# Kernel tuning notes

Measured on AMD Instinct MI355X. Metric: run time of the kernel, lower is better.

The kernel has to match this reference:

```python
import jax, jax.numpy as jnp
import numpy as np

NH = 32          # num_attention_heads
LAYER_ID = 3     # per-layer scaling coeff = LAYER_ID + 1
SQ, B, H = 1024, 2, 4096
MEM_LEN = 1024
HD = H // NH


def setup_inputs() -> dict:
    key = jax.random.key(0)
    ks = jax.random.split(key, 6)
    hidden_states = jax.random.normal(ks[0], (SQ, B, H), dtype=jnp.float32)
    mem = jax.random.normal(ks[1], (B, MEM_LEN, 2 * NH * HD), dtype=jnp.float32) * 0.5
    qkv_w = jax.random.normal(ks[2], (3 * H, H), dtype=jnp.float32) * 0.02
    qkv_b = jax.random.normal(ks[3], (3 * H,), dtype=jnp.float32) * 0.02
    dense_w = jax.random.normal(ks[4], (H, H), dtype=jnp.float32) * 0.02
    dense_b = jax.random.normal(ks[5], (H,), dtype=jnp.float32) * 0.02
    # causal mask over new tokens; mem positions fully visible. True = masked.
    kv = MEM_LEN + SQ
    mask = ((jnp.arange(kv)[None, :] - MEM_LEN) > jnp.arange(SQ)[:, None])
    mask = mask[None, None, :, :]  # [1,1,sq,kv]
    # position ids of new tokens continue after the mem cache: [b, sq]
    position_ids = jnp.broadcast_to(MEM_LEN + jnp.arange(SQ, dtype=jnp.int64), (B, SQ))
    return {"hidden_states": hidden_states, "mask": mask, "position_ids": position_ids,
            "mem": mem, "qkv_w": qkv_w, "qkv_b": qkv_b, "dense_w": dense_w, "dense_b": dense_b}


def _rotate_half(x):
    x1, x2 = jnp.split(x, 2, axis=-1)
    return jnp.concatenate((-x2, x1), axis=-1)


def _rotary_tables(max_pos):
    inv_freq = 1.0 / (10000.0 ** (jnp.arange(0, HD, 2, dtype=jnp.float32) / HD))
    t = jnp.arange(max_pos, dtype=jnp.float32)
    freqs = jnp.einsum('i,j->ij', t, inv_freq)          # [L, HD/2]
    emb = jnp.concatenate((freqs, freqs), axis=-1)      # [L, HD]
    return jnp.cos(emb), jnp.sin(emb)


def reference(hidden_states, mask, position_ids, mem, qkv_w, qkv_b, dense_w, dense_b):
    sq, b, h = hidden_states.shape
    coeff = float(LAYER_ID + 1)
    # QKV projection: [sq,b,3H] -> [sq,b,nh,3*hd] -> split
    mixed = jnp.einsum('sbh,oh->sbo', hidden_states, qkv_w) + qkv_b
    mixed = mixed.reshape(sq, b, NH, 3 * HD)
    q, k, v = jnp.split(mixed, 3, axis=-1)              # each [sq,b,nh,hd]
    # rotary embedding with position indices (position_ids: [b,sq] -> [sq,b])
    pos = position_ids.T                                 # [sq,b]
    cos_t, sin_t = _rotary_tables(MEM_LEN + SQ)          # table up to max pos + 1
    cos = cos_t[pos][:, :, None, :]                      # [sq,b,1,hd]
    sin = sin_t[pos][:, :, None, :]
    q = q * cos + _rotate_half(q) * sin
    k = k * cos + _rotate_half(k) * sin
    # mem-KV concat: mem [b, mem_len, 2*nh*hd] -> memk/memv [mem_len,b,nh,hd]
    m = mem.reshape(b, MEM_LEN, 2, NH, HD).transpose(2, 1, 0, 3, 4)
    k = jnp.concatenate((m[0], k), axis=0)               # [kv,b,nh,hd]
    v = jnp.concatenate((m[1], v), axis=0)
    # per-layer scaled attention scores
    q = q / (np.sqrt(HD) * coeff)
    scores = jnp.einsum('sbnh,tbnh->bnst', q, k)         # [b,nh,sq,kv]
    scores = jnp.where(mask, -10000.0, scores)
    scores = scores * coeff
    probs = jax.nn.softmax(scores, axis=-1)
    ctx = jnp.einsum('bnst,tbnh->sbnh', probs, v).reshape(sq, b, h)
    out = jnp.einsum('sbh,oh->sbo', ctx, dense_w) + dense_b
    return out
```

## Files before the change

### kernel.cpp

```cpp
#include <hip/hip_runtime.h>


typedef __attribute__((ext_vector_type(4))) float f32x4;
typedef __attribute__((ext_vector_type(8))) short bf16x8;
typedef unsigned short u16;

#define SQ   1024
#define BSZ  2
#define H    4096
#define NH   32
#define HD   128
#define MEML 1024
#define KV   2048

__device__ __forceinline__ u16 f32_to_bf16(float f) {
  union { float f; unsigned int u; } v; v.f = f;
  unsigned int r = v.u + 0x7FFFu + ((v.u >> 16) & 1u);
  return (u16)(r >> 16);
}
__device__ __forceinline__ float bf16_to_f32(u16 x) {
  union { unsigned int u; float f; } v; v.u = ((unsigned int)x) << 16; return v.f;
}

__device__ __forceinline__ void gload_lds16(const void* g, void* l) {
  __builtin_amdgcn_global_load_lds((const __attribute__((address_space(1))) void*)g,
                                   (__attribute__((address_space(3))) void*)l, 16, 0, 0);
}

__global__ __launch_bounds__(256) void conv_bf16(const float* __restrict__ in,
                                                 u16* __restrict__ out, int n4) {
  int idx = blockIdx.x * 256 + threadIdx.x;
  if (idx < n4) {
    float4 v = ((const float4*)in)[idx];
    ushort4 o;
    o.x = f32_to_bf16(v.x); o.y = f32_to_bf16(v.y);
    o.z = f32_to_bf16(v.z); o.w = f32_to_bf16(v.w);
    ((ushort4*)out)[idx] = o;
  }
}

__global__ __launch_bounds__(256) void rope_tables(float* __restrict__ cost, float* __restrict__ sint) {
  int idx = blockIdx.x * 256 + threadIdx.x;
  int s = idx >> 6, j = idx & 63;
  float inv = powf(10000.0f, -(float)j / 64.0f);
  float ang = (float)(MEML + s) * inv;
  cost[idx] = cosf(ang);
  sint[idx] = sinf(ang);
}

template <typename OUT_T, int NF>
__global__ __launch_bounds__(512, 2) void gemmT(const u16* __restrict__ A, const u16* __restrict__ B,
                                                const float* __restrict__ bias, OUT_T* __restrict__ C,
                                                int N, int K) {
  constexpr int WN = NF * 16;
  constexpr int NH0 = (NF + 1) / 2;
  constexpr int SB2 = NF - (NF >> 1);
  __shared__ char lds[2][32768 + NF * 8192];
  const int tid = threadIdx.x;
  const int lane = tid & 63;
  const int w = tid >> 6;
  const int wm = w >> 2, wn = w & 3;
  const int rl = lane & 15, cg = lane >> 4;
  const int m0 = blockIdx.y * 256, n0 = blockIdx.x * (NF * 64);
  const int nt = K >> 6;

  const int srow = tid >> 3;
  const int scb = ((tid & 7) << 4) ^ ((srow & 7) << 4);

  auto stage_a = [&](int tile, int ua) {
    if (tile >= nt) return;
    gload_lds16((const char*)(A + (size_t)(m0 + ua * 64 + srow) * K + (size_t)tile * 64) + scb,
                lds[tile & 1] + ua * 8192 + tid * 16);
  };
  auto stage_b = [&](int tile, int ub) {
    if (tile >= nt) return;
    gload_lds16((const char*)(B + (size_t)(n0 + ub * 64 + srow) * K + (size_t)tile * 64) + scb,
                lds[tile & 1] + 32768 + ub * 8192 + tid * 16);
  };

  f32x4 acc[8][NF];
#pragma unroll
  for (int i = 0; i < 8; ++i)
#pragma unroll
    for (int j = 0; j < NF; ++j) acc[i][j] = (f32x4){0.f, 0.f, 0.f, 0.f};

  bf16x8 af[4][2], bf[NF][2];

  auto read_a = [&](const char* buf, int mh) {
#pragma unroll
    for (int mi = 0; mi < 4; ++mi) {
      int R = wm * 128 + mh * 64 + mi * 16 + rl;
#pragma unroll
      for (int kk = 0; kk < 2; ++kk) {
        int cb = (kk * 64 + cg * 16) ^ ((R & 7) << 4);
        af[mi][kk] = *(const bf16x8*)(buf + R * 128 + cb);
      }
    }
  };
  auto read_b1 = [&](const char* buf, int nl) {
    int R = wn * WN + nl * 16 + rl;
#pragma unroll
    for (int kk = 0; kk < 2; ++kk) {
      int cb = (kk * 64 + cg * 16) ^ ((R & 7) << 4);
      bf[nl][kk] = *(const bf16x8*)(buf + 32768 + R * 128 + cb);
    }
  };
  auto mfset = [&](int mh, int lo, int hi) {
    __builtin_amdgcn_s_setprio(1);
#pragma unroll
    for (int kk = 0; kk < 2; ++kk)
#pragma unroll
      for (int mi = 0; mi < 4; ++mi)
#pragma unroll
        for (int nl = 0; nl < NF; ++nl)
          if (nl >= lo && nl < hi)
            acc[mh * 4 + mi][nl] = __builtin_amdgcn_mfma_f32_16x16x32_bf16(
                af[mi][kk], bf[nl][kk], acc[mh * 4 + mi][nl], 0, 0, 0);
    __builtin_amdgcn_s_setprio(0);
  };

#pragma unroll
  for (int ua = 0; ua < 4; ++ua) stage_a(0, ua);
#pragma unroll
  for (int ub = 0; ub < NF; ++ub) stage_b(0, ub);
#pragma unroll
  for (int ub = 0; ub < NF; ++ub) stage_b(1, ub);
  if (NF == 2)      { asm volatile("s_waitcnt vmcnt(2)" ::: "memory"); }
  else if (NF == 3) { asm volatile("s_waitcnt vmcnt(3)" ::: "memory"); }
  else              { asm volatile("s_waitcnt vmcnt(4)" ::: "memory"); }
  __builtin_amdgcn_s_barrier();

  for (int kt = 0; kt < nt; ++kt) {
    const char* buf = lds[kt & 1];
    read_a(buf, 0);
#pragma unroll
    for (int nl = 0; nl < NH0; ++nl) read_b1(buf, nl);
    stage_a(kt + 1, 0); stage_a(kt + 1, 1);
    __builtin_amdgcn_s_barrier();
    asm volatile("s_waitcnt lgkmcnt(0)" ::: "memory");
    mfset(0, 0, NH0);
    __builtin_amdgcn_s_barrier();
#pragma unroll
    for (int nl = NH0; nl < NF; ++nl) read_b1(buf, nl);
    stage_a(kt + 1, 2); stage_a(kt + 1, 3);
    __builtin_amdgcn_s_barrier();
    asm volatile("s_waitcnt lgkmcnt(0)" ::: "memory");
    mfset(0, NH0, NF);
    __builtin_amdgcn_s_barrier();
    read_a(buf, 1);
#pragma unroll
    for (int ub = 0; ub < SB2; ++ub) stage_b(kt + 2, ub);
    __builtin_amdgcn_s_barrier();
    asm volatile("s_waitcnt lgkmcnt(0)" ::: "memory");
    mfset(1, NH0, NF);
    __builtin_amdgcn_s_barrier();
#pragma unroll
    for (int ub = SB2; ub < NF; ++ub) stage_b(kt + 2, ub);
    __builtin_amdgcn_s_barrier();
    mfset(1, 0, NH0);
    if (kt + 2 < nt) {
      if (NF == 2)      { asm volatile("s_waitcnt vmcnt(2)" ::: "memory"); }
      else if (NF == 3) { asm volatile("s_waitcnt vmcnt(3)" ::: "memory"); }
      else              { asm volatile("s_waitcnt vmcnt(4)" ::: "memory"); }
    } else if (kt + 1 < nt) {
      asm volatile("s_waitcnt vmcnt(0)" ::: "memory");
    }
    __builtin_amdgcn_s_barrier();
  }

#pragma unroll
  for (int ni = 0; ni < NF; ++ni) {
    int col = n0 + wn * WN + ni * 16 + rl;
    float bv = bias[col];
#pragma unroll
    for (int mi = 0; mi < 8; ++mi) {
      int rbase = m0 + wm * 128 + mi * 16 + cg * 4;
#pragma unroll
      for (int j = 0; j < 4; ++j) {
        float v = acc[mi][ni][j] + bv;
        if constexpr (sizeof(OUT_T) == 2)
          C[(size_t)(rbase + j) * N + col] = (OUT_T)f32_to_bf16(v);
        else
          C[(size_t)(rbase + j) * N + col] = (OUT_T)v;
      }
    }
  }
}

__global__ __launch_bounds__(256) void prep_qk(const u16* __restrict__ mixed,
                                               const float* __restrict__ cost,
                                               const float* __restrict__ sint,
                                               u16* __restrict__ Qb, u16* __restrict__ Kb) {
  int s0 = blockIdx.x * 64, head = blockIdx.y;
  int b = head >> 5, nh = head & 31;
  int tid = threadIdx.x;
  const float qs = 0.08838834764831845f;
#pragma unroll
  for (int i = 0; i < 16; ++i) {
    int flat = i * 256 + tid;
    int sl = flat >> 6, j = flat & 63;
    int s = s0 + sl;
    size_t base = ((size_t)(s * 2 + b)) * 12288 + (size_t)nh * 384;
    float q1 = bf16_to_f32(mixed[base + j]),       q2 = bf16_to_f32(mixed[base + j + 64]);
    float k1 = bf16_to_f32(mixed[base + 128 + j]), k2 = bf16_to_f32(mixed[base + 192 + j]);
    float c = cost[s * 64 + j], sn = sint[s * 64 + j];
    float q1r = q1 * c - q2 * sn, q2r = q2 * c + q1 * sn;
    float k1r = k1 * c - k2 * sn, k2r = k2 * c + k1 * sn;
    size_t qoff = ((size_t)head * SQ + s) * HD;
    Qb[qoff + j]      = f32_to_bf16(q1r * qs);
    Qb[qoff + j + 64] = f32_to_bf16(q2r * qs);
    size_t koff = ((size_t)head * KV + MEML + s) * HD;
    Kb[koff + j]      = f32_to_bf16(k1r);
    Kb[koff + j + 64] = f32_to_bf16(k2r);
  }
}

__global__ __launch_bounds__(256) void prep_kv(const u16* __restrict__ mixed,
                                               const float* __restrict__ mem,
                                               u16* __restrict__ Kb, u16* __restrict__ Vtb) {
  int t0 = blockIdx.x * 64, head = blockIdx.y;
  int b = head >> 5, nh = head & 31;
  __shared__ u16 vt[128 * 72];
  int tid = threadIdx.x;
  if (t0 < MEML) {
#pragma unroll
    for (int i = 0; i < 32; ++i) {
      int flat = i * 256 + tid;
      int tl = flat >> 7, d = flat & 127;
      float kvv = mem[((size_t)b * MEML + t0 + tl) * 8192 + (size_t)nh * HD + d];
      Kb[((size_t)head * KV + t0 + tl) * HD + d] = f32_to_bf16(kvv);
    }
  }
#pragma unroll
  for (int i = 0; i < 32; ++i) {
    int flat = i * 256 + tid;
    int tl = flat >> 7, d = flat & 127;
    int t = t0 + tl;
    u16 v;
    if (t < MEML) v = f32_to_bf16(mem[((size_t)b * MEML + t) * 8192 + 4096 + (size_t)nh * HD + d]);
    else          v = mixed[((size_t)((t - MEML) * 2 + b)) * 12288 + (size_t)nh * 384 + 256 + d];
    vt[d * 72 + tl] = v;
  }
  __syncthreads();
#pragma unroll
  for (int i = 0; i < 4; ++i) {
    int c = i * 256 + tid;
    int d = c >> 3, slot = c & 7;
    *(bf16x8*)(Vtb + ((size_t)head * HD + d) * KV + t0 + slot * 8) =
        *(const bf16x8*)(vt + d * 72 + slot * 8);
  }
}

__global__ __launch_bounds__(256) void attn_fwd(const u16* __restrict__ Qb, const u16* __restrict__ Kb,
                                                const u16* __restrict__ Vtb, u16* __restrict__ ctx) {
  __shared__ u16 Ks[64 * 128];
  __shared__ u16 Vts[128 * 64];
  __shared__ u16 Ps[4 * 16 * 64];
  const int tid = threadIdx.x;
  const int lane = tid & 63;
  const int w = tid >> 6;
  const int q0 = blockIdx.x * 64;
  const int head = blockIdx.y;
  const int rl = lane & 15, cg = lane >> 4;

  bf16x8 qf[4];
  {
    const u16* Qrow = Qb + ((size_t)head * SQ + q0 + w * 16 + rl) * HD;
#pragma unroll
    for (int kk = 0; kk < 4; ++kk)
      qf[kk] = *(const bf16x8*)(Qrow + kk * 32 + cg * 8);
  }

  f32x4 acc[8];
#pragma unroll
  for (int i = 0; i < 8; ++i) acc[i] = (f32x4){0.f, 0.f, 0.f, 0.f};
  float mrow[4] = {-3.0e38f, -3.0e38f, -3.0e38f, -3.0e38f};
  float lrow[4] = {0.f, 0.f, 0.f, 0.f};

  const int t_end = q0 + 64 + MEML;

  for (int t0 = 0; t0 < t_end; t0 += 64) {
#pragma unroll
    for (int i = 0; i < 4; ++i) {
      int flat = i * 256 + tid;
      int row = flat >> 4;
      int cb = (flat & 15) << 4;
      int scb = cb ^ ((row & 7) << 4);
      gload_lds16((const char*)(Kb + ((size_t)head * KV + t0 + row) * HD) + scb,
                  (char*)Ks + (flat << 4));
    }
#pragma unroll
    for (int i = 0; i < 4; ++i) {
      int flat = i * 256 + tid;
      int row = flat >> 3;
      int cb = (flat & 7) << 4;
      int scb = cb ^ ((row & 7) << 4);
      gload_lds16((const char*)(Vtb + ((size_t)head * HD + row) * KV + t0) + scb,
                  (char*)Vts + (flat << 4));
    }
    __syncthreads();

    f32x4 sf[4];
#pragma unroll
    for (int tn = 0; tn < 4; ++tn) {
      f32x4 s = (f32x4){0.f, 0.f, 0.f, 0.f};
#pragma unroll
      for (int kk = 0; kk < 4; ++kk) {
        int row = tn * 16 + rl;
        int cb = (kk * 64 + cg * 16) ^ ((row & 7) << 4);
        bf16x8 kf = *(const bf16x8*)((const char*)Ks + row * 256 + cb);
        s = __builtin_amdgcn_mfma_f32_16x16x32_bf16(qf[kk], kf, s, 0, 0, 0);
      }
      sf[tn] = s;
    }
    if (t0 + 63 > MEML + q0 + w * 16) {
#pragma unroll
      for (int tn = 0; tn < 4; ++tn)
#pragma unroll
        for (int j = 0; j < 4; ++j) {
          int t = t0 + tn * 16 + rl;
          int srow = q0 + w * 16 + cg * 4 + j;
          if (t - MEML > srow) sf[tn][j] = -40000.0f;
        }
    }
    float mt[4];
#pragma unroll
    for (int j = 0; j < 4; ++j)
      mt[j] = fmaxf(fmaxf(sf[0][j], sf[1][j]), fmaxf(sf[2][j], sf[3][j]));
#pragma unroll
    for (int off = 1; off <= 8; off <<= 1)
#pragma unroll
      for (int j = 0; j < 4; ++j) mt[j] = fmaxf(mt[j], __shfl_xor(mt[j], off, 64));
    float pscale[4];
#pragma unroll
    for (int j = 0; j < 4; ++j) {
      float mn = fmaxf(mrow[j], mt[j]);
      pscale[j] = __expf(mrow[j] - mn);
      mrow[j] = mn;
    }
    float lsum[4] = {0.f, 0.f, 0.f, 0.f};
#pragma unroll
    for (int tn = 0; tn < 4; ++tn)
#pragma unroll
      for (int j = 0; j < 4; ++j) {
        float p = __expf(sf[tn][j] - mrow[j]);
        lsum[j] += p;
        int prow = cg * 4 + j;
        int colb = (tn * 16 + rl) * 2;
        int addr = w * 2048 + prow * 128 + (colb ^ ((prow & 7) << 4));
        *(u16*)((char*)Ps + addr) = f32_to_bf16(p);
      }
#pragma unroll
    for (int off = 1; off <= 8; off <<= 1)
#pragma unroll
      for (int j = 0; j < 4; ++j) lsum[j] += __shfl_xor(lsum[j], off, 64);
#pragma unroll
    for (int j = 0; j < 4; ++j) lrow[j] = lrow[j] * pscale[j] + lsum[j];
#pragma unroll
    for (int dn = 0; dn < 8; ++dn)
#pragma unroll
      for (int j = 0; j < 4; ++j) acc[dn][j] *= pscale[j];
#pragma unroll
    for (int dn = 0; dn < 8; ++dn) {
#pragma unroll
      for (int kk2 = 0; kk2 < 2; ++kk2) {
        int pcb = (kk2 * 64 + cg * 16) ^ ((rl & 7) << 4);
        bf16x8 pf = *(const bf16x8*)((const char*)Ps + w * 2048 + rl * 128 + pcb);
        int vrow = dn * 16 + rl;
        int vcb = (kk2 * 64 + cg * 16) ^ ((vrow & 7) << 4);
        bf16x8 vf = *(const bf16x8*)((const char*)Vts + vrow * 128 + vcb);
        acc[dn] = __builtin_amdgcn_mfma_f32_16x16x32_bf16(pf, vf, acc[dn], 0, 0, 0);
      }
    }
    __syncthreads();
  }
  const int b = head >> 5, nh = head & 31;
#pragma unroll
  for (int dn = 0; dn < 8; ++dn)
#pragma unroll
    for (int j = 0; j < 4; ++j) {
      int srow = q0 + w * 16 + cg * 4 + j;
      float v = acc[dn][j] / lrow[j];
      ctx[((size_t)(srow * 2 + b)) * H + (size_t)nh * HD + dn * 16 + rl] = f32_to_bf16(v);
    }
}

extern "C" void kernel_launch(void* const* d_in, const int* in_sizes, int n_in,
                              void* d_out, int out_size, void* d_ws, size_t ws_size,
                              hipStream_t stream) {
  const float* hidden  = (const float*)d_in[0];
  const float* mem     = (const float*)d_in[3];
  const float* qkv_w   = (const float*)d_in[4];
  const float* qkv_b   = (const float*)d_in[5];
  const float* dense_w = (const float*)d_in[6];
  const float* dense_b = (const float*)d_in[7];
  float* out = (float*)d_out;
  char* ws = (char*)d_ws;

  u16* mixed = (u16*)ws;
  char* R1 = ws + 100663296;
  u16* hid_bf = (u16*)R1;
  u16* qw_bf  = (u16*)(R1 + 16777216);
  u16* Qb  = (u16*)R1;
  u16* Kb  = (u16*)(R1 + 16777216);
  u16* Vtb = (u16*)(R1 + 50331648);
  u16* ctx = (u16*)(R1 + 83886080);
  u16* dw_bf = (u16*)(R1 + 100663296);
  float* cost = (float*)(ws + 234881024);
  float* sint = (float*)(ws + 234881024 + 262144);

  conv_bf16<<<8192, 256, 0, stream>>>(hidden, hid_bf, 2097152);
  conv_bf16<<<49152, 256, 0, stream>>>(qkv_w, qw_bf, 12582912);
  rope_tables<<<256, 256, 0, stream>>>(cost, sint);
  gemmT<u16, 3><<<dim3(64, 8), 512, 0, stream>>>(hid_bf, qw_bf, qkv_b, mixed, 12288, 4096);
  prep_qk<<<dim3(16, 64), 256, 0, stream>>>(mixed, cost, sint, Qb, Kb);
  prep_kv<<<dim3(32, 64), 256, 0, stream>>>(mixed, mem, Kb, Vtb);
  conv_bf16<<<16384, 256, 0, stream>>>(dense_w, dw_bf, 4194304);
  attn_fwd<<<dim3(16, 64), 256, 0, stream>>>(Qb, Kb, Vtb, ctx);
  gemmT<float, 2><<<dim3(32, 8), 512, 0, stream>>>(ctx, dw_bf, dense_b, out, 4096, 4096);
}
```

Measured before the change: 562.3 us.

## Double-buffer K/V tiles in attention with 128-row query blocks and 8 waves

The attention kernel now handles 128 query rows per block with 512 threads (8 waves), so each K/V tile loaded into LDS is reused by twice as many rows. K/V tiles are double-buffered: the next tile's async loads are issued before the current one is computed, using explicit vmcnt waits and raw barriers. Waves whose rows are entirely masked for a tile skip its compute. The cost is more LDS per block, fewer blocks in the grid (512), and more causal imbalance inside each block.

```diff
diff --git a/kernel.cpp b/kernel.cpp
--- a/kernel.cpp
+++ b/kernel.cpp
@@ -251,15 +251,15 @@
   }
 }
 
-__global__ __launch_bounds__(256) void attn_fwd(const u16* __restrict__ Qb, const u16* __restrict__ Kb,
+__global__ __launch_bounds__(512) void attn_fwd(const u16* __restrict__ Qb, const u16* __restrict__ Kb,
                                                 const u16* __restrict__ Vtb, u16* __restrict__ ctx) {
-  __shared__ u16 Ks[64 * 128];
-  __shared__ u16 Vts[128 * 64];
-  __shared__ u16 Ps[4 * 16 * 64];
+  __shared__ u16 Ks[2][64 * 128];
+  __shared__ u16 Vts[2][128 * 64];
+  __shared__ u16 Ps[8 * 16 * 64];
   const int tid = threadIdx.x;
   const int lane = tid & 63;
   const int w = tid >> 6;
-  const int q0 = blockIdx.x * 64;
+  const int q0 = blockIdx.x * 128;
   const int head = blockIdx.y;
   const int rl = lane & 15, cg = lane >> 4;
 
@@ -277,103 +277,120 @@
   float mrow[4] = {-3.0e38f, -3.0e38f, -3.0e38f, -3.0e38f};
   float lrow[4] = {0.f, 0.f, 0.f, 0.f};
 
-  const int t_end = q0 + 64 + MEML;
-
-  for (int t0 = 0; t0 < t_end; t0 += 64) {
-#pragma unroll
-    for (int i = 0; i < 4; ++i) {
-      int flat = i * 256 + tid;
+  const int ntile = (MEML + q0 + 128) >> 6;
+
+  auto stageKV = [&](int it) {
+    int t0 = it * 64;
+    int buf = it & 1;
+#pragma unroll
+    for (int i = 0; i < 2; ++i) {
+      int flat = i * 512 + tid;
       int row = flat >> 4;
-      int cb = (flat & 15) << 4;
-      int scb = cb ^ ((row & 7) << 4);
+      int scb = ((flat & 15) << 4) ^ ((row & 7) << 4);
       gload_lds16((const char*)(Kb + ((size_t)head * KV + t0 + row) * HD) + scb,
-                  (char*)Ks + (flat << 4));
-    }
-#pragma unroll
-    for (int i = 0; i < 4; ++i) {
-      int flat = i * 256 + tid;
+                  (char*)Ks[buf] + (flat << 4));
+    }
+#pragma unroll
+    for (int i = 0; i < 2; ++i) {
+      int flat = i * 512 + tid;
       int row = flat >> 3;
-      int cb = (flat & 7) << 4;
-      int scb = cb ^ ((row & 7) << 4);
+      int scb = ((flat & 7) << 4) ^ ((row & 7) << 4);
       gload_lds16((const char*)(Vtb + ((size_t)head * HD + row) * KV + t0) + scb,
-                  (char*)Vts + (flat << 4));
-    }
-    __syncthreads();
-
-    f32x4 sf[4];
-#pragma unroll
-    for (int tn = 0; tn < 4; ++tn) {
-      f32x4 s = (f32x4){0.f, 0.f, 0.f, 0.f};
-#pragma unroll
-      for (int kk = 0; kk < 4; ++kk) {
-        int row = tn * 16 + rl;
-        int cb = (kk * 64 + cg * 16) ^ ((row & 7) << 4);
-        bf16x8 kf = *(const bf16x8*)((const char*)Ks + row * 256 + cb);
-        s = __builtin_amdgcn_mfma_f32_16x16x32_bf16(qf[kk], kf, s, 0, 0, 0);
-      }
-      sf[tn] = s;
-    }
-    if (t0 + 63 > MEML + q0 + w * 16) {
+                  (char*)Vts[buf] + (flat << 4));
+    }
+  };
+
+  stageKV(0);
+
+  for (int it = 0; it < ntile; ++it) {
+    const int t0 = it * 64;
+    if (it + 1 < ntile) {
+      stageKV(it + 1);
+      asm volatile("s_waitcnt vmcnt(4)" ::: "memory");
+    } else {
+      asm volatile("s_waitcnt vmcnt(0)" ::: "memory");
+    }
+    __builtin_amdgcn_s_barrier();
+    const char* Kbuf = (const char*)Ks[it & 1];
+    const char* Vbuf = (const char*)Vts[it & 1];
+    const bool live = (t0 - MEML) <= (q0 + w * 16 + 15);
+    if (live) {
+      f32x4 sf[4];
+#pragma unroll
+      for (int tn = 0; tn < 4; ++tn) {
+        f32x4 s = (f32x4){0.f, 0.f, 0.f, 0.f};
+#pragma unroll
+        for (int kk = 0; kk < 4; ++kk) {
+          int row = tn * 16 + rl;
+          int cb = (kk * 64 + cg * 16) ^ ((row & 7) << 4);
+          bf16x8 kf = *(const bf16x8*)(Kbuf + row * 256 + cb);
+          s = __builtin_amdgcn_mfma_f32_16x16x32_bf16(qf[kk], kf, s, 0, 0, 0);
+        }
+        sf[tn] = s;
+      }
+      if (t0 + 63 > MEML + q0 + w * 16) {
+#pragma unroll
+        for (int tn = 0; tn < 4; ++tn)
+#pragma unroll
+          for (int j = 0; j < 4; ++j) {
+            int t = t0 + tn * 16 + rl;
+            int srow = q0 + w * 16 + cg * 4 + j;
+            if (t - MEML > srow) sf[tn][j] = -40000.0f;
+          }
+      }
+      float mt[4];
+#pragma unroll
+      for (int j = 0; j < 4; ++j)
+        mt[j] = fmaxf(fmaxf(sf[0][j], sf[1][j]), fmaxf(sf[2][j], sf[3][j]));
+#pragma unroll
+      for (int off = 1; off <= 8; off <<= 1)
+#pragma unroll
+        for (int j = 0; j < 4; ++j) mt[j] = fmaxf(mt[j], __shfl_xor(mt[j], off, 64));
+      float pscale[4];
+#pragma unroll
+      for (int j = 0; j < 4; ++j) {
+        float mn = fmaxf(mrow[j], mt[j]);
+        pscale[j] = __expf(mrow[j] - mn);
+        mrow[j] = mn;
+      }
+      float lsum[4] = {0.f, 0.f, 0.f, 0.f};
 #pragma unroll
       for (int tn = 0; tn < 4; ++tn)
 #pragma unroll
         for (int j = 0; j < 4; ++j) {
-          int t = t0 + tn * 16 + rl;
-          int srow = q0 + w * 16 + cg * 4 + j;
-          if (t - MEML > srow) sf[tn][j] = -40000.0f;
+          float p = __expf(sf[tn][j] - mrow[j]);
+          lsum[j] += p;
+          int prow = cg * 4 + j;
+          int colb = (tn * 16 + rl) * 2;
+          int addr = w * 2048 + prow * 128 + (colb ^ ((prow & 7) << 4));
+          *(u16*)((char*)Ps + addr) = f32_to_bf16(p);
         }
-    }
-    float mt[4];
-#pragma unroll
-    for (int j = 0; j < 4; ++j)
-      mt[j] = fmaxf(fmaxf(sf[0][j], sf[1][j]), fmaxf(sf[2][j], sf[3][j]));
-#pragma unroll
-    for (int off = 1; off <= 8; off <<= 1)
-#pragma unroll
-      for (int j = 0; j < 4; ++j) mt[j] = fmaxf(mt[j], __shfl_xor(mt[j], off, 64));
-    float pscale[4];
-#pragma unroll
-    for (int j = 0; j < 4; ++j) {
-      float mn = fmaxf(mrow[j], mt[j]);
-      pscale[j] = __expf(mrow[j] - mn);
-      mrow[j] = mn;
-    }
-    float lsum[4] = {0.f, 0.f, 0.f, 0.f};
-#pragma unroll
-    for (int tn = 0; tn < 4; ++tn)
-#pragma unroll
-      for (int j = 0; j < 4; ++j) {
-        float p = __expf(sf[tn][j] - mrow[j]);
-        lsum[j] += p;
-        int prow = cg * 4 + j;
-        int colb = (tn * 16 + rl) * 2;
-        int addr = w * 2048 + prow * 128 + (colb ^ ((prow & 7) << 4));
-        *(u16*)((char*)Ps + addr) = f32_to_bf16(p);
-      }
-#pragma unroll
-    for (int off = 1; off <= 8; off <<= 1)
-#pragma unroll
-      for (int j = 0; j < 4; ++j) lsum[j] += __shfl_xor(lsum[j], off, 64);
-#pragma unroll
-    for (int j = 0; j < 4; ++j) lrow[j] = lrow[j] * pscale[j] + lsum[j];
-#pragma unroll
-    for (int dn = 0; dn < 8; ++dn)
-#pragma unroll
-      for (int j = 0; j < 4; ++j) acc[dn][j] *= pscale[j];
-#pragma unroll
-    for (int dn = 0; dn < 8; ++dn) {
-#pragma unroll
-      for (int kk2 = 0; kk2 < 2; ++kk2) {
-        int pcb = (kk2 * 64 + cg * 16) ^ ((rl & 7) << 4);
-        bf16x8 pf = *(const bf16x8*)((const char*)Ps + w * 2048 + rl * 128 + pcb);
-        int vrow = dn * 16 + rl;
-        int vcb = (kk2 * 64 + cg * 16) ^ ((vrow & 7) << 4);
-        bf16x8 vf = *(const bf16x8*)((const char*)Vts + vrow * 128 + vcb);
-        acc[dn] = __builtin_amdgcn_mfma_f32_16x16x32_bf16(pf, vf, acc[dn], 0, 0, 0);
-      }
-    }
-    __syncthreads();
-  }
+#pragma unroll
+      for (int off = 1; off <= 8; off <<= 1)
+#pragma unroll
+        for (int j = 0; j < 4; ++j) lsum[j] += __shfl_xor(lsum[j], off, 64);
+#pragma unroll
+      for (int j = 0; j < 4; ++j) lrow[j] = lrow[j] * pscale[j] + lsum[j];
+#pragma unroll
+      for (int dn = 0; dn < 8; ++dn)
+#pragma unroll
+        for (int j = 0; j < 4; ++j) acc[dn][j] *= pscale[j];
+#pragma unroll
+      for (int dn = 0; dn < 8; ++dn) {
+#pragma unroll
+        for (int kk2 = 0; kk2 < 2; ++kk2) {
+          int pcb = (kk2 * 64 + cg * 16) ^ ((rl & 7) << 4);
+          bf16x8 pf = *(const bf16x8*)((const char*)Ps + w * 2048 + rl * 128 + pcb);
+          int vrow = dn * 16 + rl;
+          int vcb = (kk2 * 64 + cg * 16) ^ ((vrow & 7) << 4);
+          bf16x8 vf = *(const bf16x8*)(Vbuf + vrow * 128 + vcb);
+          acc[dn] = __builtin_amdgcn_mfma_f32_16x16x32_bf16(pf, vf, acc[dn], 0, 0, 0);
+        }
+      }
+    }
+    __builtin_amdgcn_s_barrier();
+  }
+
   const int b = head >> 5, nh = head & 31;
 #pragma unroll
   for (int dn = 0; dn < 8; ++dn)
@@ -416,6 +433,6 @@
   prep_qk<<<dim3(16, 64), 256, 0, stream>>>(mixed, cost, sint, Qb, Kb);
   prep_kv<<<dim3(32, 64), 256, 0, stream>>>(mixed, mem, Kb, Vtb);
   conv_bf16<<<16384, 256, 0, stream>>>(dense_w, dw_bf, 4194304);
-  attn_fwd<<<dim3(16, 64), 256, 0, stream>>>(Qb, Kb, Vtb, ctx);
+  attn_fwd<<<dim3(8, 64), 512, 0, stream>>>(Qb, Kb, Vtb, ctx);
   gemmT<float, 2><<<dim3(32, 8), 512, 0, stream>>>(ctx, dw_bf, dense_b, out, 4096, 4096);
 }
```

Result: no change. 563.0 us (+0.1%).
